# Kernel tuning notes

Measured on AMD Instinct MI355X. Metric: run time of the kernel, lower is better.

The kernel has to match this reference:

```python
import jax, jax.numpy as jnp
import numpy as np
import math

PHI = (1.0 + math.sqrt(5.0)) / 2.0
BASE_FAST = PHI
BASE_SLOW = 1618.0
D = 1024
NH = 16
HD = D // NH
H_GATE = max(8, D // 4)
B, L = 2, 2048


def _rope_cos_sin(seq_len, dim, base):
    # dim assumed even here (D=1024)
    idx = jnp.arange(0, dim, 2, dtype=jnp.float32) / float(dim)
    inv = 1.0 / (base ** idx)
    t = jnp.arange(seq_len, dtype=jnp.float32)
    freqs = jnp.outer(t, inv)                      # (L, dim/2)
    emb = jnp.concatenate([freqs, freqs], axis=-1) # (L, dim)
    return jnp.cos(emb), jnp.sin(emb)


def _rotate_half(x):
    d = x.shape[-1]
    x1, x2 = x[..., : d // 2], x[..., d // 2 :]
    return jnp.concatenate([-x2, x1], axis=-1)


def setup_inputs() -> dict:
    key = jax.random.key(0)
    ks = jax.random.split(key, 16)
    std = 0.02
    inp = {
        "z": jax.random.normal(ks[0], (B, L, D), jnp.float32),
        "pool_seq": jax.random.normal(ks[1], (B, L, D), jnp.float32),
        "Wq": std * jax.random.normal(ks[2], (D, D), jnp.float32),
        "bq": jnp.zeros((D,), jnp.float32),
        "Wk": std * jax.random.normal(ks[3], (D, D), jnp.float32),
        "bk": jnp.zeros((D,), jnp.float32),
        "Wv": std * jax.random.normal(ks[4], (D, D), jnp.float32),
        "bv": jnp.zeros((D,), jnp.float32),
        "W_coh": std * jax.random.normal(ks[5], (D, D), jnp.float32),
        "gamma": jnp.zeros((1,), jnp.float32) + 0.1,  # nonzero so bias path is exercised
        "Wg1": std * jax.random.normal(ks[6], (H_GATE, D), jnp.float32),
        "bg1": jnp.zeros((H_GATE,), jnp.float32),
        "Wg2": std * jax.random.normal(ks[7], (1, H_GATE), jnp.float32),
        "bg2": jnp.zeros((1,), jnp.float32),
    }
    return inp


def reference(z, pool_seq, Wq, bq, Wk, bk, Wv, bv, W_coh, gamma, Wg1, bg1, Wg2, bg2):
    b, l, d = z.shape
    # QKV projections (torch Linear: x @ W^T + b)
    Q = z @ Wq.T + bq
    K_raw = z @ Wk.T + bk
    V = z @ Wv.T + bv

    # Global coherence bias: per-query pool vector dotted with every key
    gk = pool_seq @ W_coh.T                                   # (B,L,D)
    gb = jnp.einsum("bqd,bkd->bqk", gk, K_raw) * (d ** -0.5)  # (B,L,L)
    gb = jnp.tanh(gamma[0]) * gb

    # Per-position RoPE interpolation gate (exact GELU as in torch default)
    h = jax.nn.gelu(pool_seq @ Wg1.T + bg1, approximate=False)
    gate = jax.nn.sigmoid(h @ Wg2.T + bg2)                    # (B,L,1)

    cos_f, sin_f = _rope_cos_sin(l, d, BASE_FAST)             # (L,D)
    cos_s, sin_s = _rope_cos_sin(l, d, BASE_SLOW)
    cos = gate * cos_f + (1.0 - gate) * cos_s                 # (B,L,D)
    sin = gate * sin_f + (1.0 - gate) * sin_s

    Q = Q * cos + _rotate_half(Q) * sin
    K_rot = K_raw * cos + _rotate_half(K_raw) * sin

    nh, hd = NH, d // NH
    Q_h = Q.reshape(b, l, nh, hd).transpose(0, 2, 1, 3)       # (B,H,L,hd)
    K_h = K_rot.reshape(b, l, nh, hd).transpose(0, 2, 1, 3)
    V_h = V.reshape(b, l, nh, hd).transpose(0, 2, 1, 3)

    logits = jnp.einsum("bhqd,bhkd->bhqk", Q_h, K_h) * (hd ** -0.5)
    logits = logits + gb[:, None]                             # broadcast over heads

    causal = jnp.tril(jnp.ones((l, l), dtype=bool))
    logits = jnp.where(causal[None, None], logits, -jnp.inf)

    attn_w_h = jax.nn.softmax(logits, axis=-1)                # (B,H,L,L)
    out_h = jnp.einsum("bhqk,bhkd->bhqd", attn_w_h, V_h)
    out = out_h.transpose(0, 2, 1, 3).reshape(b, l, d)
    attn_w = attn_w_h.mean(axis=1)                            # (B,L,L)
    return out, attn_w
```

## Files before the change

kernel.cpp:

```cpp
#include <hip/hip_runtime.h>
#include <hip/hip_bf16.h>

constexpr int Bn  = 2;
constexpr int Ln  = 2048;
constexpr int Dn  = 1024;
constexpr int NH  = 16;
constexpr int HGn = 256;
constexpr long BLD = (long)Bn * Ln * Dn;

typedef float f32x4 __attribute__((ext_vector_type(4)));
typedef float f32x2 __attribute__((ext_vector_type(2)));
typedef short s16x8 __attribute__((ext_vector_type(8)));
typedef short s16x4 __attribute__((ext_vector_type(4)));
typedef short s16x2 __attribute__((ext_vector_type(2)));

#define DEVI static __device__ __forceinline__

DEVI float bf2f(short u) {
  union { float f; unsigned int i; } v; v.i = ((unsigned int)(unsigned short)u) << 16; return v.f;
}
DEVI short f2bf(float f) {
  union { float f; unsigned int i; } v; v.f = f;
  unsigned int r = v.i + 0x7FFFu + ((v.i >> 16) & 1u);
  return (short)(r >> 16);
}
DEVI void gl_lds16(const void* g, void* l) {
  __builtin_amdgcn_global_load_lds((const __attribute__((address_space(1))) unsigned int*)g,
                                   (__attribute__((address_space(3))) unsigned int*)l, 16, 0, 0);
}

struct CastDesc { const float* src[7]; long cum[8]; };
__global__ void k_cast7(CastDesc d, short* __restrict__ dst) {
  long gi = ((long)blockIdx.x * 256 + threadIdx.x) * 4;
  int s = 0;
#pragma unroll
  for (int i = 1; i < 7; ++i) if (gi >= d.cum[i]) s = i;
  const float* sp = d.src[s] + (gi - d.cum[s]);
  f32x4 v = *(const f32x4*)sp;
  s16x4 o; o[0] = f2bf(v[0]); o[1] = f2bf(v[1]); o[2] = f2bf(v[2]); o[3] = f2bf(v[3]);
  *(s16x4*)(dst + gi) = o;
}

__global__ __launch_bounds__(256, 6)
void k_gemm_mega(const short* __restrict__ zb, const short* __restrict__ pb,
                 const short* __restrict__ Wcat,
                 const float* __restrict__ bq, const float* __restrict__ bk,
                 const float* __restrict__ bv, const float* __restrict__ bg1,
                 short* __restrict__ Qp, short* __restrict__ Kp,
                 short* __restrict__ Vtb, short* __restrict__ Gk,
                 short* __restrict__ Hfb) {
  int wgid = blockIdx.x;
  int xcd = wgid & 7, idx = wgid >> 3;
  int n0 = (idx >> 2) * 64;
  int m0 = (xcd * 4 + (idx & 3)) * 128;
  const short* Ap = (n0 < 3072) ? zb : pb;
  __shared__ short smA[2][128 * 32];
  __shared__ short smB[2][64 * 32];
  int tid = threadIdx.x;
  int lane = tid & 63, wid = tid >> 6;
  int wr = wid >> 1, wc = wid & 1;
  int lr = lane & 15, lg = lane >> 4;
  int r_in = lane >> 2;
  int slot = (lane & 3) * 8;
  int scol = ((lane & 3) ^ ((lane >> 3) & 3)) * 8;
  int rsw = (lr >> 1) & 3;
  f32x4 acc[4][2] = {};
  auto stage = [&](int buf, int k0) {
    int rowA = wid * 32 + r_in;
    gl_lds16(Ap   + (long)(m0 + rowA)      * Dn + k0 + scol, &smA[buf][rowA * 32 + slot]);
    gl_lds16(Ap   + (long)(m0 + rowA + 16) * Dn + k0 + scol, &smA[buf][(rowA + 16) * 32 + slot]);
    int rowB = wid * 16 + r_in;
    gl_lds16(Wcat + (long)(n0 + rowB)      * Dn + k0 + scol, &smB[buf][rowB * 32 + slot]);
  };
  stage(0, 0);
  int cur = 0;
  for (int k0 = 0; k0 < Dn; k0 += 32) {
    bool pre = (k0 + 32 < Dn);
    if (pre) stage(cur ^ 1, k0 + 32);
    __builtin_amdgcn_sched_barrier(0);
    if (pre) asm volatile("s_waitcnt vmcnt(3)" ::: "memory");
    else     asm volatile("s_waitcnt vmcnt(0)" ::: "memory");
    __builtin_amdgcn_s_barrier();
    __builtin_amdgcn_sched_barrier(0);
    const short* Ab = &smA[cur][(wr * 64 + lr) * 32 + ((lg ^ rsw) * 8)];
    const short* Bb = &smB[cur][(wc * 32 + lr) * 32 + ((lg ^ rsw) * 8)];
    s16x8 b0 = *(const s16x8*)(Bb);
    s16x8 b1 = *(const s16x8*)(Bb + 16 * 32);
#pragma unroll
    for (int m = 0; m < 4; m++) {
      s16x8 a = *(const s16x8*)(Ab + m * 16 * 32);
      acc[m][0] = __builtin_amdgcn_mfma_f32_16x16x32_bf16(a, b0, acc[m][0], 0, 0, 0);
      acc[m][1] = __builtin_amdgcn_mfma_f32_16x16x32_bf16(a, b1, acc[m][1], 0, 0, 0);
    }
    __builtin_amdgcn_s_barrier();
    cur ^= 1;
  }
  int slice = n0 >> 10;
#pragma unroll
  for (int n = 0; n < 2; n++) {
    int col = n0 + wc * 32 + n * 16 + lr;
    int c = col - (slice << 10);
    float bias = (slice == 0) ? bq[c] : (slice == 1) ? bk[c] : (slice == 2) ? bv[c]
               : (slice == 3) ? 0.0f : bg1[c];
#pragma unroll
    for (int m = 0; m < 4; m++) {
#pragma unroll
      for (int r = 0; r < 4; r++) {
        long row = m0 + wr * 64 + m * 16 + lg * 4 + r;
        float v = acc[m][n][r] + bias;
        if (slice == 4) {
          v = 0.5f * v * (1.0f + erff(v * 0.70710678118f));
          Hfb[row * HGn + c] = f2bf(v);
        } else if (slice == 2) {
          long off = (((row >> 11) * (long)NH + (c >> 6)) * 64 + (c & 63)) * Ln + (row & (Ln - 1));
          Vtb[off] = f2bf(v);
        } else {
          short* dst = (slice == 0) ? Qp : (slice == 1) ? Kp : Gk;
          dst[row * (long)Dn + c] = f2bf(v);
        }
      }
    }
  }
}

__global__ __launch_bounds__(256, 6)
void k_gemm_gbd(const short* __restrict__ A, const short* __restrict__ B,
                const float* __restrict__ gamma, short* __restrict__ C) {
  int bz = blockIdx.y;
  int t0 = blockIdx.x;
  int qp = (int)((sqrtf(4.0f * (float)t0 + 1.0f) - 1.0f) * 0.5f);
  while ((qp + 1) * (qp + 2) <= t0) ++qp;
  while (qp * (qp + 1) > t0) --qp;
  int kp = t0 - qp * (qp + 1);
  int m0 = qp * 128, n0 = kp * 64;
  const short* Ap = A + (long)bz * Ln * Dn;
  const short* Bp = B + (long)bz * Ln * Dn;
  __shared__ short smA[2][128 * 32];
  __shared__ short smB[2][64 * 32];
  int tid = threadIdx.x;
  int lane = tid & 63, wid = tid >> 6;
  int wr = wid >> 1, wc = wid & 1;
  int lr = lane & 15, lg = lane >> 4;
  int r_in = lane >> 2;
  int slot = (lane & 3) * 8;
  int scol = ((lane & 3) ^ ((lane >> 3) & 3)) * 8;
  int rsw = (lr >> 1) & 3;
  f32x4 acc[4][2] = {};
  auto stage = [&](int buf, int k0) {
    int rowA = wid * 32 + r_in;
    gl_lds16(Ap + (long)(m0 + rowA)      * Dn + k0 + scol, &smA[buf][rowA * 32 + slot]);
    gl_lds16(Ap + (long)(m0 + rowA + 16) * Dn + k0 + scol, &smA[buf][(rowA + 16) * 32 + slot]);
    int rowB = wid * 16 + r_in;
    gl_lds16(Bp + (long)(n0 + rowB)      * Dn + k0 + scol, &smB[buf][rowB * 32 + slot]);
  };
  stage(0, 0);
  int cur = 0;
  for (int k0 = 0; k0 < Dn; k0 += 32) {
    bool pre = (k0 + 32 < Dn);
    if (pre) stage(cur ^ 1, k0 + 32);
    __builtin_amdgcn_sched_barrier(0);
    if (pre) asm volatile("s_waitcnt vmcnt(3)" ::: "memory");
    else     asm volatile("s_waitcnt vmcnt(0)" ::: "memory");
    __builtin_amdgcn_s_barrier();
    __builtin_amdgcn_sched_barrier(0);
    const short* Ab = &smA[cur][(wr * 64 + lr) * 32 + ((lg ^ rsw) * 8)];
    const short* Bb = &smB[cur][(wc * 32 + lr) * 32 + ((lg ^ rsw) * 8)];
    s16x8 b0 = *(const s16x8*)(Bb);
    s16x8 b1 = *(const s16x8*)(Bb + 16 * 32);
#pragma unroll
    for (int m = 0; m < 4; m++) {
      s16x8 a = *(const s16x8*)(Ab + m * 16 * 32);
      acc[m][0] = __builtin_amdgcn_mfma_f32_16x16x32_bf16(a, b0, acc[m][0], 0, 0, 0);
      acc[m][1] = __builtin_amdgcn_mfma_f32_16x16x32_bf16(a, b1, acc[m][1], 0, 0, 0);
    }
    __builtin_amdgcn_s_barrier();
    cur ^= 1;
  }
  float alpha = tanhf(gamma[0]) * 0.03125f;
#pragma unroll
  for (int n = 0; n < 2; n++) {
    int col = n0 + wc * 32 + n * 16 + lr;
#pragma unroll
    for (int m = 0; m < 4; m++) {
#pragma unroll
      for (int r = 0; r < 4; r++) {
        long row = m0 + wr * 64 + m * 16 + lg * 4 + r;
        C[(long)bz * Ln * Ln + row * Ln + col] = f2bf(acc[m][n][r] * alpha);
      }
    }
  }
}

__global__ __launch_bounds__(256)
void k_rope_fused(short* __restrict__ Q, short* __restrict__ Kx,
                  const short* __restrict__ Hfb,
                  const float* __restrict__ Wg2, const float* __restrict__ bg2) {
  __shared__ float smG;
  int bl = blockIdx.x;
  int l = bl & (Ln - 1);
  int t = threadIdx.x;
  if (t < 64) {
    s16x4 h4 = *(const s16x4*)(Hfb + (long)bl * HGn + t * 4);
    f32x4 w = *(const f32x4*)(Wg2 + t * 4);
    float s = bf2f(h4[0]) * w[0] + bf2f(h4[1]) * w[1] + bf2f(h4[2]) * w[2] + bf2f(h4[3]) * w[3];
#pragma unroll
    for (int m = 1; m < 64; m <<= 1) s += __shfl_xor(s, m);
    if (t == 0) smG = 1.0f / (1.0f + __expf(-(s + bg2[0])));
  }
  __syncthreads();
  float g = smG;
  int j = t * 2;
  float e0 = (float)j * (1.0f / 512.0f);
  float e1 = (float)(j + 1) * (1.0f / 512.0f);
  float invf0 = powf(1.6180339887498949f, -e0);
  float invf1 = powf(1.6180339887498949f, -e1);
  float invs0 = powf(1618.0f, -e0);
  float invs1 = powf(1618.0f, -e1);
  float lf = (float)l;
  float sf0, cf0, sf1, cf1, ss0, cs0, ss1, cs1;
  sincosf(lf * invf0, &sf0, &cf0);
  sincosf(lf * invf1, &sf1, &cf1);
  sincosf(lf * invs0, &ss0, &cs0);
  sincosf(lf * invs1, &ss1, &cs1);
  float c0 = g * cf0 + (1.f - g) * cs0;
  float c1 = g * cf1 + (1.f - g) * cs1;
  float s0 = g * sf0 + (1.f - g) * ss0;
  float s1 = g * sf1 + (1.f - g) * ss1;
  long base = (long)bl * Dn + j;
  {
    s16x2 xa = *(const s16x2*)(Q + base);
    s16x2 xb = *(const s16x2*)(Q + base + 512);
    float a0 = bf2f(xa[0]), a1 = bf2f(xa[1]), b0 = bf2f(xb[0]), b1 = bf2f(xb[1]);
    s16x2 o0, o1;
    o0[0] = f2bf(a0 * c0 - b0 * s0); o0[1] = f2bf(a1 * c1 - b1 * s1);
    o1[0] = f2bf(b0 * c0 + a0 * s0); o1[1] = f2bf(b1 * c1 + a1 * s1);
    *(s16x2*)(Q + base) = o0;
    *(s16x2*)(Q + base + 512) = o1;
  }
  {
    s16x2 xa = *(const s16x2*)(Kx + base);
    s16x2 xb = *(const s16x2*)(Kx + base + 512);
    float a0 = bf2f(xa[0]), a1 = bf2f(xa[1]), b0 = bf2f(xb[0]), b1 = bf2f(xb[1]);
    s16x2 o0, o1;
    o0[0] = f2bf(a0 * c0 - b0 * s0); o0[1] = f2bf(a1 * c1 - b1 * s1);
    o1[0] = f2bf(b0 * c0 + a0 * s0); o1[1] = f2bf(b1 * c1 + a1 * s1);
    *(s16x2*)(Kx + base) = o0;
    *(s16x2*)(Kx + base + 512) = o1;
  }
}

__global__ __launch_bounds__(256)
void k_attn1(const short* __restrict__ Q, const short* __restrict__ Kx,
             const short* __restrict__ Vt, const short* __restrict__ Gb,
             float* __restrict__ outp, float* __restrict__ zinv) {
  int wg = blockIdx.x;
  int xcd = wg & 7, slot = wg >> 3;
  int p = slot & 15, gh = slot >> 4;
  int g = gh * 8 + xcd;
  int b = g >> 4, h = g & 15;

  int tid = threadIdx.x;
  int lane = tid & 63, w = tid >> 6;
  int lr = lane & 15, lg = lane >> 4;
  __shared__ short smK[2][64 * 64];
  __shared__ short smV[2][64 * 64];
  __shared__ short smP[4 * 16 * 64];
  short* pw = smP + w * 1024;

  int r0 = w * 16 + (lane >> 3);
  int scol = ((lane & 7) ^ (lane >> 3)) * 8;
  const short* Kg = Kx + (long)(b * Ln) * Dn + h * 64;
  const short* Vg = Vt + (long)(b * NH + h) * 64 * Ln;
  int sw = (lr & 7) << 3;

  for (int seg = 0; seg < 2; ++seg) {
    int qb = seg ? (31 - p) : p;
    int q0w = qb * 64 + w * 16;
    const short* qbp = Q + ((long)(b * Ln) + q0w + lr) * Dn + h * 64 + lg * 8;
    s16x8 qf0 = *(const s16x8*)(qbp);
    s16x8 qf1 = *(const s16x8*)(qbp + 32);
    f32x4 acc[4] = {};
    float az[4] = {0.f, 0.f, 0.f, 0.f};
    const short* gbase = Gb + ((long)b * Ln + q0w + lg * 4) * Ln + lr;

    int nt = qb + 1;
    auto stage = [&](int buf, int t) {
      long k0 = (long)t * 64;
      short* bK = &smK[buf][w * 1024];
      short* bV = &smV[buf][w * 1024];
      gl_lds16(Kg + (k0 + r0) * Dn + scol,           bK);
      gl_lds16(Kg + (k0 + r0 + 8) * Dn + scol,       bK + 512);
      gl_lds16(Vg + (long)r0 * Ln + k0 + scol,       bV);
      gl_lds16(Vg + (long)(r0 + 8) * Ln + k0 + scol, bV + 512);
    };

    float gcur[4][4], gnxt[4][4];
    stage(0, 0);
    {
      const short* g0 = gbase;
#pragma unroll
      for (int kk = 0; kk < 4; ++kk)
#pragma unroll
        for (int r = 0; r < 4; ++r) gcur[kk][r] = bf2f(g0[(long)r * Ln + kk * 16]);
    }
    int cur = 0;
    for (int t = 0; t < nt; ++t) {
      bool pre = (t + 1 < nt);
      if (pre) {
        const short* g0 = gbase + (t + 1) * 64;
#pragma unroll
        for (int kk = 0; kk < 4; ++kk)
#pragma unroll
          for (int r = 0; r < 4; ++r) gnxt[kk][r] = bf2f(g0[(long)r * Ln + kk * 16]);
        stage(cur ^ 1, t + 1);
      }
      __builtin_amdgcn_sched_barrier(0);
      if (pre) asm volatile("s_waitcnt vmcnt(20)" ::: "memory");
      else     asm volatile("s_waitcnt vmcnt(0)" ::: "memory");
      __builtin_amdgcn_s_barrier();
      __builtin_amdgcn_sched_barrier(0);
      int k0 = t * 64;
      const short* Kc = smK[cur];
      const short* Vc = smV[cur];
#pragma unroll
      for (int kk = 0; kk < 4; ++kk) {
        const short* kr = Kc + (kk * 16 + lr) * 64;
        s16x8 kf0 = *(const s16x8*)(kr + ((lg * 8) ^ sw));
        s16x8 kf1 = *(const s16x8*)(kr + ((32 + lg * 8) ^ sw));
        f32x4 S = {};
        S = __builtin_amdgcn_mfma_f32_16x16x32_bf16(qf0, kf0, S, 0, 0, 0);
        S = __builtin_amdgcn_mfma_f32_16x16x32_bf16(qf1, kf1, S, 0, 0, 0);
        int k = k0 + kk * 16 + lr;
#pragma unroll
        for (int r = 0; r < 4; r++) {
          int q = q0w + lg * 4 + r;
          float arg = (k <= q) ? (S[r] * 0.125f + gcur[kk][r]) : -80.0f;
          float pv = __expf(arg);
          az[r] += pv;
          int qq = lg * 4 + r;
          pw[qq * 64 + ((kk * 16 + lr) ^ ((qq & 7) << 3))] = f2bf(pv);
        }
      }
#pragma unroll
      for (int c = 0; c < 2; ++c) {
        s16x8 pf = *(const s16x8*)(pw + lr * 64 + ((c * 32 + lg * 8) ^ sw));
#pragma unroll
        for (int n = 0; n < 4; n++) {
          s16x8 vf = *(const s16x8*)(Vc + (n * 16 + lr) * 64 + ((c * 32 + lg * 8) ^ sw));
          acc[n] = __builtin_amdgcn_mfma_f32_16x16x32_bf16(pf, vf, acc[n], 0, 0, 0);
        }
      }
      __builtin_amdgcn_s_barrier();
      if (pre) {
#pragma unroll
        for (int kk = 0; kk < 4; ++kk)
#pragma unroll
          for (int r = 0; r < 4; ++r) gcur[kk][r] = gnxt[kk][r];
      }
      cur ^= 1;
    }
#pragma unroll
    for (int r = 0; r < 4; r++) {
      float z = az[r];
      z += __shfl_xor(z, 1); z += __shfl_xor(z, 2); z += __shfl_xor(z, 4); z += __shfl_xor(z, 8);
      az[r] = 1.0f / z;
    }
    if (lr == 0) {
#pragma unroll
      for (int r = 0; r < 4; r++)
        zinv[((long)(b * NH + h)) * Ln + q0w + lg * 4 + r] = az[r];
    }
#pragma unroll
    for (int n = 0; n < 4; n++) {
#pragma unroll
      for (int r = 0; r < 4; r++) {
        int q = q0w + lg * 4 + r;
        outp[((long)(b * Ln) + q) * Dn + h * 64 + n * 16 + lr] = acc[n][r] * az[r];
      }
    }
  }
}

__global__ __launch_bounds__(256)
void k_attn2(const short* __restrict__ Qm, const short* __restrict__ Kx,
             const short* __restrict__ Gb, const float* __restrict__ zinv, float* __restrict__ aw) {
  int b = blockIdx.y;
  int t = blockIdx.x;
  int qb = t >> 5, kb = t & 31;
  int q0 = qb * 64, k0 = kb * 64;
  int tid = threadIdx.x;
  if (kb > qb) {
    int row = tid >> 2, c4 = (tid & 3) << 4;
    float* basep = aw + ((long)b * Ln + q0 + row) * Ln + k0 + c4;
    f32x4 z = {};
    *(f32x4*)(basep) = z; *(f32x4*)(basep + 4) = z;
    *(f32x4*)(basep + 8) = z; *(f32x4*)(basep + 12) = z;
    return;
  }
  int lane = tid & 63, w = tid >> 6;
  int lr = lane & 15, lg = lane >> 4;
  int q0w = q0 + w * 16;
  bool diag = (qb == kb);
  __shared__ short smK[2][64 * 64];
  __shared__ short smQ[2][64 * 64];
  __shared__ float smZ[NH * 64];
  for (int i = tid; i < NH * 64; i += 256) {
    int h = i >> 6, qq = i & 63;
    smZ[i] = zinv[((long)(b * NH + h)) * Ln + q0 + qq];
  }
  __syncthreads();
  float gv[4][4];
#pragma unroll
  for (int n = 0; n < 4; n++) {
    int k = k0 + n * 16 + lr;
#pragma unroll
    for (int r = 0; r < 4; r++)
      gv[n][r] = bf2f(Gb[((long)b * Ln + q0w + lg * 4 + r) * Ln + k]);
  }
  int r0 = w * 16 + (lane >> 3);
  int scol = ((lane & 7) ^ (lane >> 3)) * 8;
  int sw = (lr & 7) << 3;
  auto stage = [&](int buf, int h) {
    short* bK = &smK[buf][w * 1024];
    short* bQ = &smQ[buf][w * 1024];
    const short* Kg = Kx + ((long)(b * Ln) + k0 + r0) * Dn + h * 64 + scol;
    gl_lds16(Kg, bK);
    gl_lds16(Kg + 8 * Dn, bK + 512);
    const short* Qg = Qm + ((long)(b * Ln) + q0 + r0) * Dn + h * 64 + scol;
    gl_lds16(Qg, bQ);
    gl_lds16(Qg + 8 * Dn, bQ + 512);
  };
  float wa[4][4] = {{0.f}};
  stage(0, 0);
  int cur = 0;
  for (int h = 0; h < NH; ++h) {
    bool pre = (h + 1 < NH);
    if (pre) stage(cur ^ 1, h + 1);
    __builtin_amdgcn_sched_barrier(0);
    if (pre) asm volatile("s_waitcnt vmcnt(4)" ::: "memory");
    else     asm volatile("s_waitcnt vmcnt(0)" ::: "memory");
    __builtin_amdgcn_s_barrier();
    __builtin_amdgcn_sched_barrier(0);
    const short* Kc = smK[cur];
    const short* Qc = smQ[cur];
    s16x8 qf0 = *(const s16x8*)(Qc + (w * 16 + lr) * 64 + ((lg * 8) ^ sw));
    s16x8 qf1 = *(const s16x8*)(Qc + (w * 16 + lr) * 64 + ((32 + lg * 8) ^ sw));
    float zq[4];
#pragma unroll
    for (int r = 0; r < 4; r++) zq[r] = smZ[h * 64 + w * 16 + lg * 4 + r];
#pragma unroll
    for (int n = 0; n < 4; n++) {
      const short* kr = Kc + (n * 16 + lr) * 64;
      s16x8 kf0 = *(const s16x8*)(kr + ((lg * 8) ^ sw));
      s16x8 kf1 = *(const s16x8*)(kr + ((32 + lg * 8) ^ sw));
      f32x4 S = {};
      S = __builtin_amdgcn_mfma_f32_16x16x32_bf16(qf0, kf0, S, 0, 0, 0);
      S = __builtin_amdgcn_mfma_f32_16x16x32_bf16(qf1, kf1, S, 0, 0, 0);
#pragma unroll
      for (int r = 0; r < 4; r++)
        wa[n][r] += __expf(S[r] * 0.125f + gv[n][r]) * zq[r];
    }
    __builtin_amdgcn_s_barrier();
    cur ^= 1;
  }
#pragma unroll
  for (int n = 0; n < 4; n++) {
    int k = k0 + n * 16 + lr;
#pragma unroll
    for (int r = 0; r < 4; r++) {
      int q = q0w + lg * 4 + r;
      float v = wa[n][r] * (1.0f / 16.0f);
      if (diag && k > q) v = 0.0f;
      aw[((long)b * Ln + q) * Ln + k] = v;
    }
  }
}

extern "C" void kernel_launch(void* const* d_in, const int* in_sizes, int n_in,
                              void* d_out, int out_size, void* d_ws, size_t ws_size,
                              hipStream_t stream) {
  const float* z    = (const float*)d_in[0];
  const float* ps   = (const float*)d_in[1];
  const float* Wq   = (const float*)d_in[2];
  const float* bq   = (const float*)d_in[3];
  const float* Wk   = (const float*)d_in[4];
  const float* bk   = (const float*)d_in[5];
  const float* Wv   = (const float*)d_in[6];
  const float* bv   = (const float*)d_in[7];
  const float* Wc   = (const float*)d_in[8];
  const float* gamma= (const float*)d_in[9];
  const float* Wg1  = (const float*)d_in[10];
  const float* bg1  = (const float*)d_in[11];
  const float* Wg2  = (const float*)d_in[12];
  const float* bg2  = (const float*)d_in[13];

  char* w = (char*)d_ws;
  auto alloc = [&](long bytes) { void* p = (void*)w; w += (bytes + 255) & ~255L; return p; };
  short* zb   = (short*)alloc(BLD * 2);
  short* pb   = (short*)alloc(BLD * 2);
  short* Wcat = (short*)alloc((long)(4 * Dn + HGn) * Dn * 2);
  short* Qp   = (short*)alloc(BLD * 2);
  short* Kp   = (short*)alloc(BLD * 2);
  short* Vtb  = (short*)alloc(BLD * 2);
  short* Gk   = (short*)alloc(BLD * 2);
  short* Hfb  = (short*)alloc((long)Bn * Ln * HGn * 2);
  float* zv   = (float*)alloc((long)Bn * NH * Ln * 4);
  short* Gb   = (short*)zb;

  float* outp = (float*)d_out;
  float* aw   = outp + BLD;

  CastDesc cd;
  cd.src[0] = z;  cd.src[1] = ps; cd.src[2] = Wq; cd.src[3] = Wk;
  cd.src[4] = Wv; cd.src[5] = Wc; cd.src[6] = Wg1;
  long c0 = 0;
  cd.cum[0] = 0;
  cd.cum[1] = (c0 += BLD);
  cd.cum[2] = (c0 += BLD);
  cd.cum[3] = (c0 += (long)Dn * Dn);
  cd.cum[4] = (c0 += (long)Dn * Dn);
  cd.cum[5] = (c0 += (long)Dn * Dn);
  cd.cum[6] = (c0 += (long)Dn * Dn);
  cd.cum[7] = (c0 += (long)HGn * Dn);
  k_cast7<<<(int)(c0 / 1024), 256, 0, stream>>>(cd, zb);

  k_gemm_mega<<<2176, 256, 0, stream>>>(zb, pb, Wcat, bq, bk, bv, bg1, Qp, Kp, Vtb, Gk, Hfb);

  k_gemm_gbd<<<dim3(272, Bn), 256, 0, stream>>>(Gk, Kp, gamma, Gb);

  k_rope_fused<<<Bn * Ln, 256, 0, stream>>>(Qp, Kp, Hfb, Wg2, bg2);

  k_attn1<<<512, 256, 0, stream>>>(Qp, Kp, Vtb, Gb, outp, zv);
  k_attn2<<<dim3(32 * 32, Bn), 256, 0, stream>>>(Qp, Kp, Gb, zv, aw);
}
```

Measured before the change: 226.6 us.

## Split attention KV tiles across two wave groups and shrink projection GEMM tiles

The attention kernel now runs 8 waves per block. Two groups of four waves process alternating key tiles, each with its own double-buffered K/V LDS. The partial accumulators and row sums are merged through LDS (reusing the second buffers) before normalisation, which raises parallelism per query block. The QKV/gate projection GEMM switches to 64x32 tiles with 2 waves and 4x as many blocks, trading operand reuse for more blocks in flight. This adds an extra LDS reduction and barriers in attention, and lowers arithmetic intensity in the GEMM.

```diff
diff --git a/kernel.cpp b/kernel.cpp
--- a/kernel.cpp
+++ b/kernel.cpp
@@ -41,7 +41,7 @@
   *(s16x4*)(dst + gi) = o;
 }
 
-__global__ __launch_bounds__(256, 6)
+__global__ __launch_bounds__(128, 8)
 void k_gemm_mega(const short* __restrict__ zb, const short* __restrict__ pb,
                  const short* __restrict__ Wcat,
                  const float* __restrict__ bq, const float* __restrict__ bk,
@@ -51,26 +51,22 @@
                  short* __restrict__ Hfb) {
   int wgid = blockIdx.x;
   int xcd = wgid & 7, idx = wgid >> 3;
-  int n0 = (idx >> 2) * 64;
-  int m0 = (xcd * 4 + (idx & 3)) * 128;
+  int n0 = (idx >> 3) * 32;
+  int m0 = (xcd * 8 + (idx & 7)) * 64;
   const short* Ap = (n0 < 3072) ? zb : pb;
-  __shared__ short smA[2][128 * 32];
-  __shared__ short smB[2][64 * 32];
+  __shared__ short smA[2][64 * 32];
+  __shared__ short smB[2][32 * 32];
   int tid = threadIdx.x;
   int lane = tid & 63, wid = tid >> 6;
-  int wr = wid >> 1, wc = wid & 1;
   int lr = lane & 15, lg = lane >> 4;
-  int r_in = lane >> 2;
-  int slot = (lane & 3) * 8;
+  int sr = lane >> 2;
   int scol = ((lane & 3) ^ ((lane >> 3) & 3)) * 8;
   int rsw = (lr >> 1) & 3;
-  f32x4 acc[4][2] = {};
+  f32x4 acc[2][2] = {};
   auto stage = [&](int buf, int k0) {
-    int rowA = wid * 32 + r_in;
-    gl_lds16(Ap   + (long)(m0 + rowA)      * Dn + k0 + scol, &smA[buf][rowA * 32 + slot]);
-    gl_lds16(Ap   + (long)(m0 + rowA + 16) * Dn + k0 + scol, &smA[buf][(rowA + 16) * 32 + slot]);
-    int rowB = wid * 16 + r_in;
-    gl_lds16(Wcat + (long)(n0 + rowB)      * Dn + k0 + scol, &smB[buf][rowB * 32 + slot]);
+    gl_lds16(Ap   + (long)(m0 + wid * 16 + sr)      * Dn + k0 + scol, &smA[buf][(wid * 16) * 32]);
+    gl_lds16(Ap   + (long)(m0 + 32 + wid * 16 + sr) * Dn + k0 + scol, &smA[buf][(32 + wid * 16) * 32]);
+    gl_lds16(Wcat + (long)(n0 + wid * 16 + sr)      * Dn + k0 + scol, &smB[buf][(wid * 16) * 32]);
   };
   stage(0, 0);
   int cur = 0;
@@ -82,12 +78,12 @@
     else     asm volatile("s_waitcnt vmcnt(0)" ::: "memory");
     __builtin_amdgcn_s_barrier();
     __builtin_amdgcn_sched_barrier(0);
-    const short* Ab = &smA[cur][(wr * 64 + lr) * 32 + ((lg ^ rsw) * 8)];
-    const short* Bb = &smB[cur][(wc * 32 + lr) * 32 + ((lg ^ rsw) * 8)];
+    const short* Ab = &smA[cur][(wid * 32 + lr) * 32 + ((lg ^ rsw) * 8)];
+    const short* Bb = &smB[cur][lr * 32 + ((lg ^ rsw) * 8)];
     s16x8 b0 = *(const s16x8*)(Bb);
     s16x8 b1 = *(const s16x8*)(Bb + 16 * 32);
 #pragma unroll
-    for (int m = 0; m < 4; m++) {
+    for (int m = 0; m < 2; m++) {
       s16x8 a = *(const s16x8*)(Ab + m * 16 * 32);
       acc[m][0] = __builtin_amdgcn_mfma_f32_16x16x32_bf16(a, b0, acc[m][0], 0, 0, 0);
       acc[m][1] = __builtin_amdgcn_mfma_f32_16x16x32_bf16(a, b1, acc[m][1], 0, 0, 0);
@@ -98,15 +94,15 @@
   int slice = n0 >> 10;
 #pragma unroll
   for (int n = 0; n < 2; n++) {
-    int col = n0 + wc * 32 + n * 16 + lr;
+    int col = n0 + n * 16 + lr;
     int c = col - (slice << 10);
     float bias = (slice == 0) ? bq[c] : (slice == 1) ? bk[c] : (slice == 2) ? bv[c]
                : (slice == 3) ? 0.0f : bg1[c];
 #pragma unroll
-    for (int m = 0; m < 4; m++) {
+    for (int m = 0; m < 2; m++) {
 #pragma unroll
       for (int r = 0; r < 4; r++) {
-        long row = m0 + wr * 64 + m * 16 + lg * 4 + r;
+        long row = m0 + wid * 32 + m * 16 + lg * 4 + r;
         float v = acc[m][n][r] + bias;
         if (slice == 4) {
           v = 0.5f * v * (1.0f + erff(v * 0.70710678118f));
@@ -249,7 +245,7 @@
   }
 }
 
-__global__ __launch_bounds__(256)
+__global__ __launch_bounds__(512)
 void k_attn1(const short* __restrict__ Q, const short* __restrict__ Kx,
              const short* __restrict__ Vt, const short* __restrict__ Gb,
              float* __restrict__ outp, float* __restrict__ zinv) {
@@ -261,13 +257,16 @@
 
   int tid = threadIdx.x;
   int lane = tid & 63, w = tid >> 6;
+  int rw = w & 3, kg = w >> 2;
   int lr = lane & 15, lg = lane >> 4;
-  __shared__ short smK[2][64 * 64];
-  __shared__ short smV[2][64 * 64];
-  __shared__ short smP[4 * 16 * 64];
+  __shared__ short smK[2][2][64 * 64];
+  __shared__ short smV[2][2][64 * 64];
+  __shared__ short smP[8 * 16 * 64];
+  float* mAcc = (float*)&smK[1][0][0];
+  float* mAz  = (float*)&smV[1][0][0];
   short* pw = smP + w * 1024;
 
-  int r0 = w * 16 + (lane >> 3);
+  int r0 = rw * 16 + (lane >> 3);
   int scol = ((lane & 7) ^ (lane >> 3)) * 8;
   const short* Kg = Kx + (long)(b * Ln) * Dn + h * 64;
   const short* Vg = Vt + (long)(b * NH + h) * 64 * Ln;
@@ -275,7 +274,9 @@
 
   for (int seg = 0; seg < 2; ++seg) {
     int qb = seg ? (31 - p) : p;
-    int q0w = qb * 64 + w * 16;
+    int nt = qb + 1;
+    int ntc = (nt + 1) >> 1;
+    int q0w = qb * 64 + rw * 16;
     const short* qbp = Q + ((long)(b * Ln) + q0w + lr) * Dn + h * 64 + lg * 8;
     s16x8 qf0 = *(const s16x8*)(qbp);
     s16x8 qf1 = *(const s16x8*)(qbp + 32);
@@ -283,11 +284,10 @@
     float az[4] = {0.f, 0.f, 0.f, 0.f};
     const short* gbase = Gb + ((long)b * Ln + q0w + lg * 4) * Ln + lr;
 
-    int nt = qb + 1;
     auto stage = [&](int buf, int t) {
       long k0 = (long)t * 64;
-      short* bK = &smK[buf][w * 1024];
-      short* bV = &smV[buf][w * 1024];
+      short* bK = &smK[kg][buf][rw * 1024];
+      short* bV = &smV[kg][buf][rw * 1024];
       gl_lds16(Kg + (k0 + r0) * Dn + scol,           bK);
       gl_lds16(Kg + (k0 + r0 + 8) * Dn + scol,       bK + 512);
       gl_lds16(Vg + (long)r0 * Ln + k0 + scol,       bV);
@@ -295,89 +295,113 @@
     };
 
     float gcur[4][4], gnxt[4][4];
-    stage(0, 0);
-    {
-      const short* g0 = gbase;
+    if (kg < nt) {
+      stage(0, kg);
+      const short* g0 = gbase + kg * 64;
 #pragma unroll
       for (int kk = 0; kk < 4; ++kk)
 #pragma unroll
         for (int r = 0; r < 4; ++r) gcur[kk][r] = bf2f(g0[(long)r * Ln + kk * 16]);
     }
     int cur = 0;
-    for (int t = 0; t < nt; ++t) {
-      bool pre = (t + 1 < nt);
+    for (int tt = 0; tt < ntc; ++tt) {
+      int t = 2 * tt + kg;
+      bool valid = (t < nt);
+      bool pre = (t + 2 < nt);
       if (pre) {
-        const short* g0 = gbase + (t + 1) * 64;
+        const short* g0 = gbase + (t + 2) * 64;
 #pragma unroll
         for (int kk = 0; kk < 4; ++kk)
 #pragma unroll
           for (int r = 0; r < 4; ++r) gnxt[kk][r] = bf2f(g0[(long)r * Ln + kk * 16]);
-        stage(cur ^ 1, t + 1);
+        stage(cur ^ 1, t + 2);
       }
       __builtin_amdgcn_sched_barrier(0);
       if (pre) asm volatile("s_waitcnt vmcnt(20)" ::: "memory");
       else     asm volatile("s_waitcnt vmcnt(0)" ::: "memory");
       __builtin_amdgcn_s_barrier();
       __builtin_amdgcn_sched_barrier(0);
-      int k0 = t * 64;
-      const short* Kc = smK[cur];
-      const short* Vc = smV[cur];
-#pragma unroll
-      for (int kk = 0; kk < 4; ++kk) {
-        const short* kr = Kc + (kk * 16 + lr) * 64;
-        s16x8 kf0 = *(const s16x8*)(kr + ((lg * 8) ^ sw));
-        s16x8 kf1 = *(const s16x8*)(kr + ((32 + lg * 8) ^ sw));
-        f32x4 S = {};
-        S = __builtin_amdgcn_mfma_f32_16x16x32_bf16(qf0, kf0, S, 0, 0, 0);
-        S = __builtin_amdgcn_mfma_f32_16x16x32_bf16(qf1, kf1, S, 0, 0, 0);
-        int k = k0 + kk * 16 + lr;
+      if (valid) {
+        int k0 = t * 64;
+        const short* Kc = smK[kg][cur];
+        const short* Vc = smV[kg][cur];
+#pragma unroll
+        for (int kk = 0; kk < 4; ++kk) {
+          const short* kr = Kc + (kk * 16 + lr) * 64;
+          s16x8 kf0 = *(const s16x8*)(kr + ((lg * 8) ^ sw));
+          s16x8 kf1 = *(const s16x8*)(kr + ((32 + lg * 8) ^ sw));
+          f32x4 S = {};
+          S = __builtin_amdgcn_mfma_f32_16x16x32_bf16(qf0, kf0, S, 0, 0, 0);
+          S = __builtin_amdgcn_mfma_f32_16x16x32_bf16(qf1, kf1, S, 0, 0, 0);
+          int k = k0 + kk * 16 + lr;
+#pragma unroll
+          for (int r = 0; r < 4; r++) {
+            int q = q0w + lg * 4 + r;
+            float arg = (k <= q) ? (S[r] * 0.125f + gcur[kk][r]) : -80.0f;
+            float pv = __expf(arg);
+            az[r] += pv;
+            int qq = lg * 4 + r;
+            pw[qq * 64 + ((kk * 16 + lr) ^ ((qq & 7) << 3))] = f2bf(pv);
+          }
+        }
+#pragma unroll
+        for (int c = 0; c < 2; ++c) {
+          s16x8 pf = *(const s16x8*)(pw + lr * 64 + ((c * 32 + lg * 8) ^ sw));
+#pragma unroll
+          for (int n = 0; n < 4; n++) {
+            s16x8 vf = *(const s16x8*)(Vc + (n * 16 + lr) * 64 + ((c * 32 + lg * 8) ^ sw));
+            acc[n] = __builtin_amdgcn_mfma_f32_16x16x32_bf16(pf, vf, acc[n], 0, 0, 0);
+          }
+        }
+      }
+      __builtin_amdgcn_s_barrier();
+      if (pre) {
+#pragma unroll
+        for (int kk = 0; kk < 4; ++kk)
+#pragma unroll
+          for (int r = 0; r < 4; ++r) gcur[kk][r] = gnxt[kk][r];
+      }
+      cur ^= 1;
+    }
+    if (kg == 1) {
+      float* da = mAcc + rw * 1024;
+#pragma unroll
+      for (int n = 0; n < 4; n++)
+#pragma unroll
+        for (int r = 0; r < 4; r++) da[lane * 16 + n * 4 + r] = acc[n][r];
+      float* dz = mAz + rw * 256;
+#pragma unroll
+      for (int r = 0; r < 4; r++) dz[lane * 4 + r] = az[r];
+    }
+    __syncthreads();
+    if (kg == 0) {
+      const float* sa = mAcc + rw * 1024;
+      const float* sz = mAz + rw * 256;
+#pragma unroll
+      for (int n = 0; n < 4; n++)
+#pragma unroll
+        for (int r = 0; r < 4; r++) acc[n][r] += sa[lane * 16 + n * 4 + r];
+#pragma unroll
+      for (int r = 0; r < 4; r++) {
+        float z = az[r] + sz[lane * 4 + r];
+        z += __shfl_xor(z, 1); z += __shfl_xor(z, 2); z += __shfl_xor(z, 4); z += __shfl_xor(z, 8);
+        az[r] = 1.0f / z;
+      }
+      if (lr == 0) {
+#pragma unroll
+        for (int r = 0; r < 4; r++)
+          zinv[((long)(b * NH + h)) * Ln + q0w + lg * 4 + r] = az[r];
+      }
+#pragma unroll
+      for (int n = 0; n < 4; n++) {
 #pragma unroll
         for (int r = 0; r < 4; r++) {
           int q = q0w + lg * 4 + r;
-          float arg = (k <= q) ? (S[r] * 0.125f + gcur[kk][r]) : -80.0f;
-          float pv = __expf(arg);
-          az[r] += pv;
-          int qq = lg * 4 + r;
-          pw[qq * 64 + ((kk * 16 + lr) ^ ((qq & 7) << 3))] = f2bf(pv);
+          outp[((long)(b * Ln) + q) * Dn + h * 64 + n * 16 + lr] = acc[n][r] * az[r];
         }
       }
-#pragma unroll
-      for (int c = 0; c < 2; ++c) {
-        s16x8 pf = *(const s16x8*)(pw + lr * 64 + ((c * 32 + lg * 8) ^ sw));
-#pragma unroll
-        for (int n = 0; n < 4; n++) {
-          s16x8 vf = *(const s16x8*)(Vc + (n * 16 + lr) * 64 + ((c * 32 + lg * 8) ^ sw));
-          acc[n] = __builtin_amdgcn_mfma_f32_16x16x32_bf16(pf, vf, acc[n], 0, 0, 0);
-        }
-      }
-      __builtin_amdgcn_s_barrier();
-      if (pre) {
-#pragma unroll
-        for (int kk = 0; kk < 4; ++kk)
-#pragma unroll
-          for (int r = 0; r < 4; ++r) gcur[kk][r] = gnxt[kk][r];
-      }
-      cur ^= 1;
-    }
-#pragma unroll
-    for (int r = 0; r < 4; r++) {
-      float z = az[r];
-      z += __shfl_xor(z, 1); z += __shfl_xor(z, 2); z += __shfl_xor(z, 4); z += __shfl_xor(z, 8);
-      az[r] = 1.0f / z;
-    }
-    if (lr == 0) {
-#pragma unroll
-      for (int r = 0; r < 4; r++)
-        zinv[((long)(b * NH + h)) * Ln + q0w + lg * 4 + r] = az[r];
-    }
-#pragma unroll
-    for (int n = 0; n < 4; n++) {
-#pragma unroll
-      for (int r = 0; r < 4; r++) {
-        int q = q0w + lg * 4 + r;
-        outp[((long)(b * Ln) + q) * Dn + h * 64 + n * 16 + lr] = acc[n][r] * az[r];
-      }
-    }
+    }
+    __syncthreads();
   }
 }
 
@@ -524,12 +548,12 @@
   cd.cum[7] = (c0 += (long)HGn * Dn);
   k_cast7<<<(int)(c0 / 1024), 256, 0, stream>>>(cd, zb);
 
-  k_gemm_mega<<<2176, 256, 0, stream>>>(zb, pb, Wcat, bq, bk, bv, bg1, Qp, Kp, Vtb, Gk, Hfb);
+  k_gemm_mega<<<8704, 128, 0, stream>>>(zb, pb, Wcat, bq, bk, bv, bg1, Qp, Kp, Vtb, Gk, Hfb);
 
   k_gemm_gbd<<<dim3(272, Bn), 256, 0, stream>>>(Gk, Kp, gamma, Gb);
 
   k_rope_fused<<<Bn * Ln, 256, 0, stream>>>(Qp, Kp, Hfb, Wg2, bg2);
 
-  k_attn1<<<512, 256, 0, stream>>>(Qp, Kp, Vtb, Gb, outp, zv);
+  k_attn1<<<512, 512, 0, stream>>>(Qp, Kp, Vtb, Gb, outp, zv);
   k_attn2<<<dim3(32 * 32, Bn), 256, 0, stream>>>(Qp, Kp, Gb, zv, aw);
 }
```

After: 276.3 us. +21.9%, slower.

## Run both causal query segments concurrently in 512-thread attention blocks

Applied to the files above, without the earlier changes.

The attention kernel previously processed two paired query blocks (p and 31-p) sequentially within a 256-thread workgroup. Now each 512-thread workgroup runs both segments at once on separate 4-wave halves, with separate K/V LDS buffers. The two halves come from different (b,h) pairs, so the grid still covers 512 blocks with twice the threads. This is meant to raise parallelism and shorten per-block latency. In exchange it doubles LDS per block, and the short segment idles at barriers while the long one finishes, since the loop runs to the longer length.

```diff
diff --git a/kernel.cpp b/kernel.cpp
--- a/kernel.cpp
+++ b/kernel.cpp
@@ -249,79 +249,88 @@
   }
 }
 
-__global__ __launch_bounds__(256)
+__global__ __launch_bounds__(512)
 void k_attn1(const short* __restrict__ Q, const short* __restrict__ Kx,
              const short* __restrict__ Vt, const short* __restrict__ Gb,
              float* __restrict__ outp, float* __restrict__ zinv) {
   int wg = blockIdx.x;
-  int xcd = wg & 7, slot = wg >> 3;
-  int p = slot & 15, gh = slot >> 4;
-  int g = gh * 8 + xcd;
-  int b = g >> 4, h = g & 15;
+  int xcd = wg & 7, rest = wg >> 3;
+  int p2 = rest & 15;
+  int jhalf = (rest >> 4) & 1;
+  int shalf = (rest >> 5) & 1;
+  int p = shalf ? (15 - p2) : p2;
+  int jj = jhalf * 8 + xcd;
 
   int tid = threadIdx.x;
   int lane = tid & 63, w = tid >> 6;
+  int seg = w >> 2, rw = w & 3;
   int lr = lane & 15, lg = lane >> 4;
-  __shared__ short smK[2][64 * 64];
-  __shared__ short smV[2][64 * 64];
-  __shared__ short smP[4 * 16 * 64];
+
+  int g = jj * 2 + ((seg ^ shalf) & 1);
+  int b = g >> 4, h = g & 15;
+  int qb = seg ? (31 - p) : p;
+  int nt = qb + 1;
+  int ntmax = 32 - p;
+  int q0w = qb * 64 + rw * 16;
+
+  __shared__ short smK[2][2][64 * 64];
+  __shared__ short smV[2][2][64 * 64];
+  __shared__ short smP[8 * 16 * 64];
   short* pw = smP + w * 1024;
 
-  int r0 = w * 16 + (lane >> 3);
+  int r0 = rw * 16 + (lane >> 3);
   int scol = ((lane & 7) ^ (lane >> 3)) * 8;
   const short* Kg = Kx + (long)(b * Ln) * Dn + h * 64;
   const short* Vg = Vt + (long)(b * NH + h) * 64 * Ln;
   int sw = (lr & 7) << 3;
 
-  for (int seg = 0; seg < 2; ++seg) {
-    int qb = seg ? (31 - p) : p;
-    int q0w = qb * 64 + w * 16;
-    const short* qbp = Q + ((long)(b * Ln) + q0w + lr) * Dn + h * 64 + lg * 8;
-    s16x8 qf0 = *(const s16x8*)(qbp);
-    s16x8 qf1 = *(const s16x8*)(qbp + 32);
-    f32x4 acc[4] = {};
-    float az[4] = {0.f, 0.f, 0.f, 0.f};
-    const short* gbase = Gb + ((long)b * Ln + q0w + lg * 4) * Ln + lr;
-
-    int nt = qb + 1;
-    auto stage = [&](int buf, int t) {
-      long k0 = (long)t * 64;
-      short* bK = &smK[buf][w * 1024];
-      short* bV = &smV[buf][w * 1024];
-      gl_lds16(Kg + (k0 + r0) * Dn + scol,           bK);
-      gl_lds16(Kg + (k0 + r0 + 8) * Dn + scol,       bK + 512);
-      gl_lds16(Vg + (long)r0 * Ln + k0 + scol,       bV);
-      gl_lds16(Vg + (long)(r0 + 8) * Ln + k0 + scol, bV + 512);
-    };
-
-    float gcur[4][4], gnxt[4][4];
-    stage(0, 0);
-    {
-      const short* g0 = gbase;
+  const short* qbp = Q + ((long)(b * Ln) + q0w + lr) * Dn + h * 64 + lg * 8;
+  s16x8 qf0 = *(const s16x8*)(qbp);
+  s16x8 qf1 = *(const s16x8*)(qbp + 32);
+  f32x4 acc[4] = {};
+  float az[4] = {0.f, 0.f, 0.f, 0.f};
+  const short* gbase = Gb + ((long)b * Ln + q0w + lg * 4) * Ln + lr;
+
+  auto stage = [&](int buf, int t) {
+    long k0 = (long)t * 64;
+    short* bK = &smK[seg][buf][rw * 1024];
+    short* bV = &smV[seg][buf][rw * 1024];
+    gl_lds16(Kg + (k0 + r0) * Dn + scol,           bK);
+    gl_lds16(Kg + (k0 + r0 + 8) * Dn + scol,       bK + 512);
+    gl_lds16(Vg + (long)r0 * Ln + k0 + scol,       bV);
+    gl_lds16(Vg + (long)(r0 + 8) * Ln + k0 + scol, bV + 512);
+  };
+
+  float gcur[4][4], gnxt[4][4];
+  stage(0, 0);
+  {
+    const short* g0 = gbase;
+#pragma unroll
+    for (int kk = 0; kk < 4; ++kk)
+#pragma unroll
+      for (int r = 0; r < 4; ++r) gcur[kk][r] = bf2f(g0[(long)r * Ln + kk * 16]);
+  }
+  int cur = 0;
+  for (int t = 0; t < ntmax; ++t) {
+    bool active = (t < nt);
+    bool pre = (t + 1 < nt);
+    if (pre) {
+      const short* g0 = gbase + (t + 1) * 64;
 #pragma unroll
       for (int kk = 0; kk < 4; ++kk)
 #pragma unroll
-        for (int r = 0; r < 4; ++r) gcur[kk][r] = bf2f(g0[(long)r * Ln + kk * 16]);
-    }
-    int cur = 0;
-    for (int t = 0; t < nt; ++t) {
-      bool pre = (t + 1 < nt);
-      if (pre) {
-        const short* g0 = gbase + (t + 1) * 64;
-#pragma unroll
-        for (int kk = 0; kk < 4; ++kk)
-#pragma unroll
-          for (int r = 0; r < 4; ++r) gnxt[kk][r] = bf2f(g0[(long)r * Ln + kk * 16]);
-        stage(cur ^ 1, t + 1);
-      }
-      __builtin_amdgcn_sched_barrier(0);
-      if (pre) asm volatile("s_waitcnt vmcnt(20)" ::: "memory");
-      else     asm volatile("s_waitcnt vmcnt(0)" ::: "memory");
-      __builtin_amdgcn_s_barrier();
-      __builtin_amdgcn_sched_barrier(0);
+        for (int r = 0; r < 4; ++r) gnxt[kk][r] = bf2f(g0[(long)r * Ln + kk * 16]);
+      stage(cur ^ 1, t + 1);
+    }
+    __builtin_amdgcn_sched_barrier(0);
+    if (pre) asm volatile("s_waitcnt vmcnt(20)" ::: "memory");
+    else     asm volatile("s_waitcnt vmcnt(0)" ::: "memory");
+    __builtin_amdgcn_s_barrier();
+    __builtin_amdgcn_sched_barrier(0);
+    if (active) {
       int k0 = t * 64;
-      const short* Kc = smK[cur];
-      const short* Vc = smV[cur];
+      const short* Kc = smK[seg][cur];
+      const short* Vc = smV[seg][cur];
 #pragma unroll
       for (int kk = 0; kk < 4; ++kk) {
         const short* kr = Kc + (kk * 16 + lr) * 64;
@@ -350,33 +359,33 @@
           acc[n] = __builtin_amdgcn_mfma_f32_16x16x32_bf16(pf, vf, acc[n], 0, 0, 0);
         }
       }
-      __builtin_amdgcn_s_barrier();
-      if (pre) {
-#pragma unroll
-        for (int kk = 0; kk < 4; ++kk)
-#pragma unroll
-          for (int r = 0; r < 4; ++r) gcur[kk][r] = gnxt[kk][r];
-      }
-      cur ^= 1;
-    }
+    }
+    __builtin_amdgcn_s_barrier();
+    if (pre) {
+#pragma unroll
+      for (int kk = 0; kk < 4; ++kk)
+#pragma unroll
+        for (int r = 0; r < 4; ++r) gcur[kk][r] = gnxt[kk][r];
+    }
+    cur ^= 1;
+  }
+#pragma unroll
+  for (int r = 0; r < 4; r++) {
+    float z = az[r];
+    z += __shfl_xor(z, 1); z += __shfl_xor(z, 2); z += __shfl_xor(z, 4); z += __shfl_xor(z, 8);
+    az[r] = 1.0f / z;
+  }
+  if (lr == 0) {
+#pragma unroll
+    for (int r = 0; r < 4; r++)
+      zinv[((long)(b * NH + h)) * Ln + q0w + lg * 4 + r] = az[r];
+  }
+#pragma unroll
+  for (int n = 0; n < 4; n++) {
 #pragma unroll
     for (int r = 0; r < 4; r++) {
-      float z = az[r];
-      z += __shfl_xor(z, 1); z += __shfl_xor(z, 2); z += __shfl_xor(z, 4); z += __shfl_xor(z, 8);
-      az[r] = 1.0f / z;
-    }
-    if (lr == 0) {
-#pragma unroll
-      for (int r = 0; r < 4; r++)
-        zinv[((long)(b * NH + h)) * Ln + q0w + lg * 4 + r] = az[r];
-    }
-#pragma unroll
-    for (int n = 0; n < 4; n++) {
-#pragma unroll
-      for (int r = 0; r < 4; r++) {
-        int q = q0w + lg * 4 + r;
-        outp[((long)(b * Ln) + q) * Dn + h * 64 + n * 16 + lr] = acc[n][r] * az[r];
-      }
+      int q = q0w + lg * 4 + r;
+      outp[((long)(b * Ln) + q) * Dn + h * 64 + n * 16 + lr] = acc[n][r] * az[r];
     }
   }
 }
@@ -530,6 +539,6 @@
 
   k_rope_fused<<<Bn * Ln, 256, 0, stream>>>(Qp, Kp, Hfb, Wg2, bg2);
 
-  k_attn1<<<512, 256, 0, stream>>>(Qp, Kp, Vtb, Gb, outp, zv);
+  k_attn1<<<512, 512, 0, stream>>>(Qp, Kp, Vtb, Gb, outp, zv);
   k_attn2<<<dim3(32 * 32, Bn), 256, 0, stream>>>(Qp, Kp, Gb, zv, aw);
 }
```

New measurement: 274.9 us. +21.3%, slower.
